# Optimization experiments

Hardware: AMD Instinct MI355X
Metric: run time of the kernel (lower is better)

Reference implementation:

```python
import jax, jax.numpy as jnp
import numpy as np

N_USER = 50000
N_ITEM = 50000
N = N_USER + N_ITEM
EMB = 64
FEAT = 64
LAYERS = [128, 128]   # input_dim = EMB + FEAT = 128
NNZ = 3_200_000
BATCH = 4096
NEG_SLOPE = 0.2
EPS = 1e-12


def setup_inputs() -> dict:
    key = jax.random.key(0)
    ks = jax.random.split(key, 16)
    inp = {}
    # forward index args
    inp["users"] = jax.random.randint(ks[0], (BATCH,), 0, N_USER)
    inp["pos_items"] = jax.random.randint(ks[1], (BATCH,), 0, N_ITEM)
    inp["neg_items"] = jax.random.randint(ks[2], (BATCH,), 0, N_ITEM)
    # learned embeddings (xavier-ish scale)
    inp["user_emb"] = jax.random.normal(ks[3], (N_USER, EMB), jnp.float32) * 0.1
    inp["item_emb1"] = jax.random.normal(ks[4], (N_ITEM, EMB), jnp.float32) * 0.1
    inp["item_emb2"] = jax.random.normal(ks[5], (N_ITEM, FEAT), jnp.float32) * 0.1
    # fixed user feature matrix (densified sparse feature, non-trainable)
    inp["feature"] = jax.random.normal(ks[6], (N_USER, FEAT), jnp.float32) * 0.1
    # hop-mixing scalar weights w1,w2,w3 (softmax(alpha) at init, then free params)
    alpha = jax.random.normal(ks[7], (3,), jnp.float32)
    inp["w"] = jax.nn.softmax(alpha)
    # per-layer GC / BI weights (all 128x128 here, so stack)
    din = EMB + FEAT
    sc = 1.0 / np.sqrt(din)
    K = len(LAYERS)
    inp["W_gc"] = jax.random.uniform(ks[8], (K, din, LAYERS[0]), jnp.float32, -sc, sc)
    inp["b_gc"] = jax.random.uniform(ks[9], (K, 1, LAYERS[0]), jnp.float32, -sc, sc)
    inp["W_bi"] = jax.random.uniform(ks[10], (K, din, LAYERS[0]), jnp.float32, -sc, sc)
    inp["b_bi"] = jax.random.uniform(ks[11], (K, 1, LAYERS[0]), jnp.float32, -sc, sc)
    # normalized adjacency in COO form (same sparsity pattern for all hops)
    inp["adj_rows"] = jax.random.randint(ks[12], (NNZ,), 0, N)
    inp["adj_cols"] = jax.random.randint(ks[13], (NNZ,), 0, N)
    inp["adj_vals"] = jax.random.uniform(ks[14], (NNZ,), jnp.float32, 0.0, 0.06)
    return inp


def _spmm(vals, rows, cols, X):
    # sparse (N,N) @ dense (N,D) via gather + segment-sum
    return jax.ops.segment_sum(vals[:, None] * X[cols], rows, num_segments=N)


def _forward(users, pos_items, neg_items, user_emb, item_emb1, item_emb2,
             feature, w, W_gc, b_gc, W_bi, b_bi, adj_rows, adj_cols, adj_vals):
    temp = jnp.concatenate([feature, item_emb2], axis=0)            # (N, FEAT)
    ego = jnp.concatenate([user_emb, item_emb1], axis=0)            # (N, EMB)
    ego = jnp.concatenate([ego, temp], axis=1)                      # (N, 128)
    all_emb = [ego]
    # torch `A ** i` cumulative -> elementwise value powers v, v^2, v^6
    v = adj_vals
    comb = w[0] * v + w[1] * (v ** 2) + w[2] * (v ** 6)
    for k in range(len(LAYERS)):
        side = _spmm(comb, adj_rows, adj_cols, ego)                 # (N, 128)
        sum_e = side @ W_gc[k] + b_gc[k]
        bi_e = (ego * side) @ W_bi[k] + b_bi[k]
        ego = jax.nn.leaky_relu(sum_e + bi_e, negative_slope=NEG_SLOPE)
        nrm = jnp.linalg.norm(ego, axis=1, keepdims=True)
        all_emb.append(ego / jnp.maximum(nrm, EPS))                 # F.normalize
    all_e = jnp.concatenate(all_emb, axis=1)                        # (N, 384)
    u_g = all_e[:N_USER][users]
    pos_g = all_e[N_USER:][pos_items]
    neg_g = all_e[N_USER:][neg_items]
    return u_g, pos_g, neg_g


def reference(users, pos_items, neg_items, user_emb, item_emb1, item_emb2,
              feature, w, W_gc, b_gc, W_bi, b_bi, adj_rows, adj_cols, adj_vals):
    return _forward(users, pos_items, neg_items, user_emb, item_emb1, item_emb2,
                    feature, w, W_gc, b_gc, W_bi, b_bi, adj_rows, adj_cols, adj_vals)
```

## Files before the change

### kernel.cpp

```cpp
#include <hip/hip_runtime.h>
#include <math.h>

#define N_USER 50000
#define N_ITEM 50000
#define NTOT   100000
#define D      128
#define BATCH_ 4096
#define NEG_SLOPE 0.2f
#define EPS_ 1e-12f
#define SCAN_CHUNK 1024
#define NBUK 782
#define NCHK 256
#define NSCAN (NBUK * NCHK)
#define BUKCAP 12288

typedef __attribute__((ext_vector_type(8))) short bfrag;
typedef __attribute__((ext_vector_type(4))) float f32x4;

static __device__ __forceinline__ float bf2f(unsigned short h) {
    return __uint_as_float(((unsigned)h) << 16);
}
static __device__ __forceinline__ unsigned short f2bf(float f) {
    unsigned u = __float_as_uint(f);
    u += 0x7fffu + ((u >> 16) & 1u);
    return (unsigned short)(u >> 16);
}

__global__ void assemble_ego0(const float* __restrict__ user_emb,
                              const float* __restrict__ item_emb1,
                              const float* __restrict__ item_emb2,
                              const float* __restrict__ feature,
                              unsigned short* __restrict__ ego0h) {
    int t = blockIdx.x * blockDim.x + threadIdx.x;
    const int total = NTOT * (D / 4);
    if (t >= total) return;
    int row = t >> 5;
    int q   = t & 31;
    int d0  = q * 4;
    const float* src;
    if (d0 < 64) {
        src = (row < N_USER) ? user_emb  + (size_t)row * 64 + d0
                             : item_emb1 + (size_t)(row - N_USER) * 64 + d0;
    } else {
        src = (row < N_USER) ? feature   + (size_t)row * 64 + (d0 - 64)
                             : item_emb2 + (size_t)(row - N_USER) * 64 + (d0 - 64);
    }
    float4 v = *(const float4*)src;
    ushort4 h;
    h.x = f2bf(v.x); h.y = f2bf(v.y); h.z = f2bf(v.z); h.w = f2bf(v.w);
    *(ushort4*)(ego0h + (size_t)row * D + d0) = h;
}

__global__ void pack_w(const float* __restrict__ W_gc, const float* __restrict__ W_bi,
                       unsigned short* __restrict__ Wp) {
    int t = blockIdx.x * blockDim.x + threadIdx.x;
    if (t >= 8192) return;
    int lane  = t & 63;
    int nt    = (t >> 6) & 7;
    int kt    = (t >> 9) & 3;
    int mat   = (t >> 11) & 1;
    int layer = (t >> 12) & 1;
    const float* W = (mat ? W_bi : W_gc) + (size_t)layer * D * D;
    int n = nt * 16 + (lane & 15);
    int kbase = kt * 32 + (lane >> 4) * 8;
    unsigned short o8[8];
    #pragma unroll
    for (int e = 0; e < 8; ++e) o8[e] = f2bf(W[(size_t)(kbase + e) * D + n]);
    *(int4*)(Wp + (size_t)t * 8) = *(int4*)o8;
}

__global__ __launch_bounds__(1024) void hist_buckets(const int* __restrict__ rows,
                                                     int* __restrict__ cnt2,
                                                     int nnz, int chunk_sz) {
    __shared__ int h[NBUK];
    for (int i = threadIdx.x; i < NBUK; i += 1024) h[i] = 0;
    __syncthreads();
    int c = blockIdx.x;
    int base = c * chunk_sz, end = min(base + chunk_sz, nnz);
    for (int e = base + threadIdx.x; e < end; e += 1024)
        atomicAdd(&h[rows[e] >> 7], 1);
    __syncthreads();
    for (int b = threadIdx.x; b < NBUK; b += 1024)
        cnt2[b * NCHK + c] = h[b];
}

__global__ __launch_bounds__(1024) void scan_block_sums(const int* __restrict__ cnt,
                                                        int* __restrict__ bsum, int n) {
    __shared__ int ws[16];
    int i = blockIdx.x * SCAN_CHUNK + threadIdx.x;
    int x = (i < n) ? cnt[i] : 0;
    #pragma unroll
    for (int d = 32; d >= 1; d >>= 1) x += __shfl_xor(x, d);
    int wid = threadIdx.x >> 6, lane = threadIdx.x & 63;
    if (lane == 0) ws[wid] = x;
    __syncthreads();
    if (threadIdx.x == 0) {
        int s = 0;
        #pragma unroll
        for (int k = 0; k < 16; ++k) s += ws[k];
        bsum[blockIdx.x] = s;
    }
}

__global__ void scan_small(const int* __restrict__ bsum, int* __restrict__ boff, int nb) {
    if (threadIdx.x == 0 && blockIdx.x == 0) {
        int acc = 0;
        for (int i = 0; i < nb; ++i) { boff[i] = acc; acc += bsum[i]; }
    }
}

__global__ __launch_bounds__(1024) void scan_chunks(const int* __restrict__ cnt,
                                                    const int* __restrict__ boff,
                                                    int* __restrict__ off, int n) {
    __shared__ int ws[16];
    int tid = threadIdx.x;
    int i = blockIdx.x * SCAN_CHUNK + tid;
    int x = (i < n) ? cnt[i] : 0;
    int v = x;
    #pragma unroll
    for (int d = 1; d < 64; d <<= 1) { int u = __shfl_up(v, d); if ((tid & 63) >= d) v += u; }
    int wid = tid >> 6, lane = tid & 63;
    if (lane == 63) ws[wid] = v;
    __syncthreads();
    if (wid == 0) {
        int s = (lane < 16) ? ws[lane] : 0;
        #pragma unroll
        for (int d = 1; d < 16; d <<= 1) { int u = __shfl_up(s, d); if (lane >= d) s += u; }
        if (lane < 16) ws[lane] = s;
    }
    __syncthreads();
    int woff = (wid == 0) ? 0 : ws[wid - 1];
    if (i < n) off[i] = boff[blockIdx.x] + woff + v - x;
}

__global__ __launch_bounds__(1024) void partition_edges(
        const int* __restrict__ rows, const int* __restrict__ cols,
        const float* __restrict__ vals, const float* __restrict__ w3,
        const int* __restrict__ scanout, int2* __restrict__ tmp8,
        int nnz, int chunk_sz) {
    __shared__ int cur[NBUK];
    int c = blockIdx.x;
    for (int b = threadIdx.x; b < NBUK; b += 1024) cur[b] = scanout[b * NCHK + c];
    __syncthreads();
    const float w0 = w3[0], w1 = w3[1], w2 = w3[2];
    int base = c * chunk_sz, end = min(base + chunk_sz, nnz);
    for (int e = base + threadIdx.x; e < end; e += 1024) {
        int r = rows[e];
        float v = vals[e];
        float v2 = v * v;
        float comb = w0 * v + w1 * v2 + w2 * v2 * v2 * v2;
        int pos = atomicAdd(&cur[r >> 7], 1);
        tmp8[pos] = make_int2(((r & 127) << 17) | cols[e], __float_as_int(comb));
    }
}

__global__ __launch_bounds__(256) void bucket_sort(
        const int2* __restrict__ tmp8, const int* __restrict__ scanout,
        unsigned* __restrict__ edges4, int* __restrict__ row_off, int nnz) {
    __shared__ int hist[128], exc[129], cur[128];
    __shared__ unsigned st[BUKCAP];
    int b = blockIdx.x;
    int lo = scanout[b * NCHK];
    int hi = (b + 1 < NBUK) ? scanout[(b + 1) * NCHK] : nnz;
    int cnt = hi - lo;
    if (threadIdx.x < 128) hist[threadIdx.x] = 0;
    __syncthreads();
    for (int i = lo + threadIdx.x; i < hi; i += 256)
        atomicAdd(&hist[tmp8[i].x >> 17], 1);
    __syncthreads();
    if (threadIdx.x == 0) {
        int a = 0;
        for (int r = 0; r < 128; ++r) { exc[r] = a; a += hist[r]; }
        exc[128] = a;
    }
    __syncthreads();
    if (threadIdx.x < 128) {
        cur[threadIdx.x] = exc[threadIdx.x];
        int grow = b * 128 + threadIdx.x;
        if (grow <= NTOT) row_off[grow] = lo + exc[threadIdx.x];
    }
    __syncthreads();
    if (cnt <= BUKCAP) {
        for (int i = lo + threadIdx.x; i < hi; i += 256) {
            int2 t = tmp8[i];
            int rl = t.x >> 17;
            int p = atomicAdd(&cur[rl], 1);
            unsigned cb = (unsigned)f2bf(__int_as_float(t.y)) & 0x7FFFu;
            st[p] = (cb << 17) | ((unsigned)t.x & 0x1FFFFu);
        }
        __syncthreads();
        for (int i = threadIdx.x; i < cnt; i += 256)
            edges4[lo + i] = st[i];
    } else {
        for (int i = lo + threadIdx.x; i < hi; i += 256) {
            int2 t = tmp8[i];
            int rl = t.x >> 17;
            int p = atomicAdd(&cur[rl], 1);
            unsigned cb = (unsigned)f2bf(__int_as_float(t.y)) & 0x7FFFu;
            edges4[lo + p] = (cb << 17) | ((unsigned)t.x & 0x1FFFFu);
        }
    }
}

__global__ __launch_bounds__(256) void spmm_csr_h(const int* __restrict__ row_off,
                                                  const unsigned* __restrict__ edges4,
                                                  const unsigned short* __restrict__ Xh,
                                                  unsigned short* __restrict__ side_h) {
    int row = (blockIdx.x * blockDim.x + threadIdx.x) >> 6;
    if (row >= NTOT) return;
    int lane = threadIdx.x & 63;
    int g = lane >> 4;
    int q = lane & 15;
    int s = row_off[row], e = row_off[row + 1];

    float a[8];
    #pragma unroll
    for (int j = 0; j < 8; ++j) a[j] = 0.f;

    for (int i = s; i < e; i += 8) {
        int i0 = i + g, i1 = i + 4 + g;
        unsigned e0 = (i0 < e) ? edges4[i0] : 0u;
        unsigned e1 = (i1 < e) ? edges4[i1] : 0u;
        float v0 = bf2f((unsigned short)(e0 >> 17));
        float v1 = bf2f((unsigned short)(e1 >> 17));
        int4 x0 = *(const int4*)(Xh + (size_t)(e0 & 0x1FFFFu) * D + q * 8);
        int4 x1 = *(const int4*)(Xh + (size_t)(e1 & 0x1FFFFu) * D + q * 8);
        const unsigned short* p0 = (const unsigned short*)&x0;
        const unsigned short* p1 = (const unsigned short*)&x1;
        #pragma unroll
        for (int j = 0; j < 8; ++j)
            a[j] += v0 * bf2f(p0[j]) + v1 * bf2f(p1[j]);
    }
    #pragma unroll
    for (int j = 0; j < 8; ++j) {
        a[j] += __shfl_xor(a[j], 16);
        a[j] += __shfl_xor(a[j], 32);
    }
    if (g == 0) {
        unsigned short o[8];
        #pragma unroll
        for (int j = 0; j < 8; ++j) o[j] = f2bf(a[j]);
        *(int4*)(side_h + (size_t)row * D + q * 8) = *(int4*)o;
    }
}

__global__ __launch_bounds__(256) void layer_gemm_mfma(
        const unsigned short* __restrict__ side_h,
        const unsigned short* __restrict__ ego_h,
        const unsigned short* __restrict__ Wp, int layer,
        const float* __restrict__ bgc, const float* __restrict__ bbi,
        unsigned short* __restrict__ ego_out_h, float* __restrict__ norms) {
    __shared__ unsigned short Sl[64 * D];
    __shared__ unsigned short Pl[64 * D];
    __shared__ float sqp[4][64];

    const int r0  = blockIdx.x * 64;
    const int tid = threadIdx.x;
    const int lane = tid & 63;
    const int wv   = tid >> 6;

    #pragma unroll
    for (int it = 0; it < 4; ++it) {
        int c = tid + it * 256;
        int r = c >> 4;
        int q = c & 15;
        int row = r0 + r;
        int4 sv = make_int4(0, 0, 0, 0), ev = make_int4(0, 0, 0, 0);
        if (row < NTOT) {
            sv = *(const int4*)(side_h + (size_t)row * D + q * 8);
            ev = *(const int4*)(ego_h  + (size_t)row * D + q * 8);
        }
        int dst = (r * 256 + q * 16) ^ ((r & 7) << 4);
        *(int4*)((char*)Sl + dst) = sv;
        const unsigned short* sp = (const unsigned short*)&sv;
        const unsigned short* ep = (const unsigned short*)&ev;
        unsigned short pv[8];
        #pragma unroll
        for (int j = 0; j < 8; ++j) pv[j] = f2bf(bf2f(sp[j]) * bf2f(ep[j]));
        *(int4*)((char*)Pl + dst) = *(int4*)pv;
    }

    bfrag wg[4][2], wb[4][2];
    #pragma unroll
    for (int kt = 0; kt < 4; ++kt)
        #pragma unroll
        for (int n2 = 0; n2 < 2; ++n2) {
            int nt = wv * 2 + n2;
            size_t og = ((((size_t)(layer * 2 + 0) * 4 + kt) * 8 + nt) * 64 + lane) * 8;
            size_t ob = ((((size_t)(layer * 2 + 1) * 4 + kt) * 8 + nt) * 64 + lane) * 8;
            wg[kt][n2] = *(const bfrag*)(Wp + og);
            wb[kt][n2] = *(const bfrag*)(Wp + ob);
        }

    __syncthreads();

    f32x4 acc[4][2];
    #pragma unroll
    for (int m = 0; m < 4; ++m)
        #pragma unroll
        for (int n = 0; n < 2; ++n) acc[m][n] = (f32x4){0.f, 0.f, 0.f, 0.f};

    #pragma unroll
    for (int kt = 0; kt < 4; ++kt) {
        bfrag sf[4], pf[4];
        #pragma unroll
        for (int m = 0; m < 4; ++m) {
            int rowl = m * 16 + (lane & 15);
            int byte = (rowl * 256 + kt * 64 + (lane >> 4) * 16) ^ ((rowl & 7) << 4);
            sf[m] = *(const bfrag*)((const char*)Sl + byte);
            pf[m] = *(const bfrag*)((const char*)Pl + byte);
        }
        #pragma unroll
        for (int m = 0; m < 4; ++m)
            #pragma unroll
            for (int n = 0; n < 2; ++n) {
                acc[m][n] = __builtin_amdgcn_mfma_f32_16x16x32_bf16(sf[m], wg[kt][n], acc[m][n], 0, 0, 0);
                acc[m][n] = __builtin_amdgcn_mfma_f32_16x16x32_bf16(pf[m], wb[kt][n], acc[m][n], 0, 0, 0);
            }
    }

    float bsum[2];
    #pragma unroll
    for (int n = 0; n < 2; ++n) {
        int col = wv * 32 + n * 16 + (lane & 15);
        bsum[n] = bgc[col] + bbi[col];
    }

    float sq[4][4];
    #pragma unroll
    for (int m = 0; m < 4; ++m)
        #pragma unroll
        for (int r = 0; r < 4; ++r) sq[m][r] = 0.f;

    #pragma unroll
    for (int m = 0; m < 4; ++m) {
        int rowl = m * 16 + (lane >> 4) * 4;
        #pragma unroll
        for (int n = 0; n < 2; ++n) {
            int col = wv * 32 + n * 16 + (lane & 15);
            #pragma unroll
            for (int r = 0; r < 4; ++r) {
                float o = acc[m][n][r] + bsum[n];
                o = (o > 0.f) ? o : NEG_SLOPE * o;
                sq[m][r] += o * o;
                int row = r0 + rowl + r;
                if (row < NTOT)
                    ego_out_h[(size_t)row * D + col] = f2bf(o);
            }
        }
    }

    #pragma unroll
    for (int m = 0; m < 4; ++m)
        #pragma unroll
        for (int r = 0; r < 4; ++r) {
            float v = sq[m][r];
            #pragma unroll
            for (int off = 8; off >= 1; off >>= 1) v += __shfl_xor(v, off);
            if ((lane & 15) == 0) sqp[wv][m * 16 + (lane >> 4) * 4 + r] = v;
        }
    __syncthreads();
    if (tid < 64) {
        int row = r0 + tid;
        if (row < NTOT) {
            float s = sqp[0][tid] + sqp[1][tid] + sqp[2][tid] + sqp[3][tid];
            norms[row] = fmaxf(sqrtf(s), EPS_);
        }
    }
}

__global__ void gather_out(const int* __restrict__ users,
                           const int* __restrict__ pos,
                           const int* __restrict__ neg,
                           const float* __restrict__ user_emb,
                           const float* __restrict__ item_emb1,
                           const float* __restrict__ item_emb2,
                           const float* __restrict__ feature,
                           const unsigned short* __restrict__ ego1h,
                           const unsigned short* __restrict__ ego2h,
                           const float* __restrict__ n1,
                           const float* __restrict__ n2,
                           float* __restrict__ out) {
    int t = blockIdx.x * blockDim.x + threadIdx.x;
    const int total = 3 * BATCH_ * 384;
    if (t >= total) return;
    int c = t % 384;
    int i = (t / 384) % BATCH_;
    int s = t / (384 * BATCH_);
    int idx  = (s == 0) ? users[i] : (s == 1 ? pos[i] : neg[i]);
    int node = (s == 0) ? idx : idx + N_USER;
    float val;
    if (c < 128) {
        if (s == 0)
            val = (c < 64) ? user_emb[(size_t)idx * 64 + c]
                           : feature[(size_t)idx * 64 + (c - 64)];
        else
            val = (c < 64) ? item_emb1[(size_t)idx * 64 + c]
                           : item_emb2[(size_t)idx * 64 + (c - 64)];
    } else if (c < 256) {
        val = bf2f(ego1h[(size_t)node * D + (c - 128)]) / n1[node];
    } else {
        val = bf2f(ego2h[(size_t)node * D + (c - 256)]) / n2[node];
    }
    out[t] = val;
}

extern "C" void kernel_launch(void* const* d_in, const int* in_sizes, int n_in,
                              void* d_out, int out_size, void* d_ws, size_t ws_size,
                              hipStream_t stream) {
    const int*   users     = (const int*)d_in[0];
    const int*   pos_items = (const int*)d_in[1];
    const int*   neg_items = (const int*)d_in[2];
    const float* user_emb  = (const float*)d_in[3];
    const float* item_emb1 = (const float*)d_in[4];
    const float* item_emb2 = (const float*)d_in[5];
    const float* feature   = (const float*)d_in[6];
    const float* w3        = (const float*)d_in[7];
    const float* W_gc      = (const float*)d_in[8];
    const float* b_gc      = (const float*)d_in[9];
    const float* W_bi      = (const float*)d_in[10];
    const float* b_bi      = (const float*)d_in[11];
    const int*   adj_rows  = (const int*)d_in[12];
    const int*   adj_cols  = (const int*)d_in[13];
    const float* adj_vals  = (const float*)d_in[14];
    const int nnz = in_sizes[14];

    const size_t nd = (size_t)NTOT * D;
    const int NB2 = (NSCAN + SCAN_CHUNK - 1) / SCAN_CHUNK;

    char* p = (char*)d_ws;
    float* n1    = (float*)p;                 p += NTOT * 4;
    float* n2    = (float*)p;                 p += NTOT * 4;
    unsigned short* ego0h  = (unsigned short*)p; p += nd * 2;
    unsigned short* ego1h  = (unsigned short*)p; p += nd * 2;
    unsigned short* ego2h  = (unsigned short*)p; p += nd * 2;
    unsigned short* side_h = (unsigned short*)p; p += nd * 2;
    unsigned short* Wp     = (unsigned short*)p; p += 8192 * 8 * 2;
    int*  row_off = (int*)p;                  p += (NTOT + 4) * 4;
    int*  cnt2    = (int*)p;                  p += (size_t)NSCAN * 4;
    int*  scanout = (int*)p;                  p += (size_t)NSCAN * 4;
    int*  bsum    = (int*)p;                  p += 256 * 4;
    int*  boff    = (int*)p;                  p += 256 * 4;
    int2* tmp8    = (int2*)p;                 p += (size_t)nnz * 8;
    unsigned* edges4 = (unsigned*)p;          p += (size_t)nnz * 4;

    float* out = (float*)d_out;

    {
        int total = NTOT * (D / 4);
        assemble_ego0<<<(total + 255) / 256, 256, 0, stream>>>(
            user_emb, item_emb1, item_emb2, feature, ego0h);
    }
    pack_w<<<8192 / 256, 256, 0, stream>>>(W_gc, W_bi, Wp);

    int chunk_sz = (nnz + NCHK - 1) / NCHK;
    hist_buckets<<<NCHK, 1024, 0, stream>>>(adj_rows, cnt2, nnz, chunk_sz);
    scan_block_sums<<<NB2, SCAN_CHUNK, 0, stream>>>(cnt2, bsum, NSCAN);
    scan_small<<<1, 64, 0, stream>>>(bsum, boff, NB2);
    scan_chunks<<<NB2, SCAN_CHUNK, 0, stream>>>(cnt2, boff, scanout, NSCAN);
    partition_edges<<<NCHK, 1024, 0, stream>>>(adj_rows, adj_cols, adj_vals, w3,
                                               scanout, tmp8, nnz, chunk_sz);
    bucket_sort<<<NBUK, 256, 0, stream>>>(tmp8, scanout, edges4, row_off, nnz);

    for (int k = 0; k < 2; ++k) {
        const unsigned short* Xh = (k == 0) ? ego0h : ego1h;
        unsigned short* egoNh    = (k == 0) ? ego1h : ego2h;
        float* nrm               = (k == 0) ? n1 : n2;

        spmm_csr_h<<<(NTOT + 3) / 4, 256, 0, stream>>>(row_off, edges4, Xh, side_h);
        layer_gemm_mfma<<<(NTOT + 63) / 64, 256, 0, stream>>>(
            side_h, Xh, Wp, k,
            b_gc + (size_t)k * D, b_bi + (size_t)k * D,
            egoNh, nrm);
    }

    {
        int total = 3 * BATCH_ * 384;
        gather_out<<<(total + 255) / 256, 256, 0, stream>>>(
            users, pos_items, neg_items,
            user_emb, item_emb1, item_emb2, feature,
            ego1h, ego2h, n1, n2, out);
    }
}
```

Measured before the change: 380.1 us.

## Fuse SpMM into layer GEMM and sort edges by column panel within rows

The separate SpMM kernel is merged into the layer GEMM kernel. Each block now gathers neighbor rows for its 64 rows and writes side and the side*ego product straight into shared memory, so the side_h round trip through global memory goes away. Separately, bucket_sort now orders edges inside each row by a column-panel key (col>>12), which groups gathers into nearby X rows for better cache locality. The sort uses more shared memory (NKEY histograms) and a halved staging buffer, which shifts more buckets onto the scattered global-write fallback. The fused kernel may also lose occupancy and parallelism because each block walks 64 rows serially.

```diff
diff --git a/kernel.cpp b/kernel.cpp
--- a/kernel.cpp
+++ b/kernel.cpp
@@ -12,7 +12,9 @@
 #define NBUK 782
 #define NCHK 256
 #define NSCAN (NBUK * NCHK)
-#define BUKCAP 12288
+#define BUKCAP 6144
+#define NPAN 25
+#define NKEY (128 * NPAN)
 
 typedef __attribute__((ext_vector_type(8))) short bfrag;
 typedef __attribute__((ext_vector_type(4))) float f32x4;
@@ -157,96 +159,78 @@
 __global__ __launch_bounds__(256) void bucket_sort(
         const int2* __restrict__ tmp8, const int* __restrict__ scanout,
         unsigned* __restrict__ edges4, int* __restrict__ row_off, int nnz) {
-    __shared__ int hist[128], exc[129], cur[128];
+    __shared__ int hist[NKEY];
+    __shared__ int cur[NKEY];
+    __shared__ int ssum[256];
+    __shared__ int wtot[4];
     __shared__ unsigned st[BUKCAP];
+    const int tid = threadIdx.x, lane = tid & 63, wv = tid >> 6;
     int b = blockIdx.x;
     int lo = scanout[b * NCHK];
     int hi = (b + 1 < NBUK) ? scanout[(b + 1) * NCHK] : nnz;
     int cnt = hi - lo;
-    if (threadIdx.x < 128) hist[threadIdx.x] = 0;
-    __syncthreads();
-    for (int i = lo + threadIdx.x; i < hi; i += 256)
-        atomicAdd(&hist[tmp8[i].x >> 17], 1);
-    __syncthreads();
-    if (threadIdx.x == 0) {
-        int a = 0;
-        for (int r = 0; r < 128; ++r) { exc[r] = a; a += hist[r]; }
-        exc[128] = a;
-    }
-    __syncthreads();
-    if (threadIdx.x < 128) {
-        cur[threadIdx.x] = exc[threadIdx.x];
-        int grow = b * 128 + threadIdx.x;
-        if (grow <= NTOT) row_off[grow] = lo + exc[threadIdx.x];
-    }
-    __syncthreads();
+
+    for (int i = tid; i < NKEY; i += 256) hist[i] = 0;
+    __syncthreads();
+    for (int i = lo + tid; i < hi; i += 256) {
+        unsigned x = (unsigned)tmp8[i].x;
+        atomicAdd(&hist[(x >> 17) * NPAN + ((x & 0x1FFFFu) >> 12)], 1);
+    }
+    __syncthreads();
+
+    const int base = tid * 13;
+    int s = 0;
+    #pragma unroll
+    for (int j = 0; j < 13; ++j) { int idx = base + j; if (idx < NKEY) s += hist[idx]; }
+    int incl = s;
+    #pragma unroll
+    for (int d = 1; d < 64; d <<= 1) { int u = __shfl_up(incl, d); if (lane >= d) incl += u; }
+    if (lane == 63) wtot[wv] = incl;
+    __syncthreads();
+    int woff = 0;
+    for (int k = 0; k < 4; ++k) if (k < wv) woff += wtot[k];
+    int acc = woff + incl - s;
+    #pragma unroll
+    for (int j = 0; j < 13; ++j) {
+        int idx = base + j;
+        if (idx < NKEY) { int h = hist[idx]; hist[idx] = acc; acc += h; }
+    }
+    __syncthreads();
+
+    for (int i = tid; i < NKEY; i += 256) cur[i] = hist[i];
+    if (tid < 128) {
+        int grow = b * 128 + tid;
+        if (grow <= NTOT) row_off[grow] = lo + hist[tid * NPAN];
+    }
+    __syncthreads();
+
     if (cnt <= BUKCAP) {
-        for (int i = lo + threadIdx.x; i < hi; i += 256) {
+        for (int i = lo + tid; i < hi; i += 256) {
             int2 t = tmp8[i];
-            int rl = t.x >> 17;
-            int p = atomicAdd(&cur[rl], 1);
+            unsigned x = (unsigned)t.x;
+            int key = (x >> 17) * NPAN + ((x & 0x1FFFFu) >> 12);
+            int p = atomicAdd(&cur[key], 1);
             unsigned cb = (unsigned)f2bf(__int_as_float(t.y)) & 0x7FFFu;
-            st[p] = (cb << 17) | ((unsigned)t.x & 0x1FFFFu);
+            st[p] = (cb << 17) | (x & 0x1FFFFu);
         }
         __syncthreads();
-        for (int i = threadIdx.x; i < cnt; i += 256)
+        for (int i = tid; i < cnt; i += 256)
             edges4[lo + i] = st[i];
     } else {
-        for (int i = lo + threadIdx.x; i < hi; i += 256) {
+        for (int i = lo + tid; i < hi; i += 256) {
             int2 t = tmp8[i];
-            int rl = t.x >> 17;
-            int p = atomicAdd(&cur[rl], 1);
+            unsigned x = (unsigned)t.x;
+            int key = (x >> 17) * NPAN + ((x & 0x1FFFFu) >> 12);
+            int p = atomicAdd(&cur[key], 1);
             unsigned cb = (unsigned)f2bf(__int_as_float(t.y)) & 0x7FFFu;
-            edges4[lo + p] = (cb << 17) | ((unsigned)t.x & 0x1FFFFu);
-        }
-    }
-}
-
-__global__ __launch_bounds__(256) void spmm_csr_h(const int* __restrict__ row_off,
-                                                  const unsigned* __restrict__ edges4,
-                                                  const unsigned short* __restrict__ Xh,
-                                                  unsigned short* __restrict__ side_h) {
-    int row = (blockIdx.x * blockDim.x + threadIdx.x) >> 6;
-    if (row >= NTOT) return;
-    int lane = threadIdx.x & 63;
-    int g = lane >> 4;
-    int q = lane & 15;
-    int s = row_off[row], e = row_off[row + 1];
-
-    float a[8];
-    #pragma unroll
-    for (int j = 0; j < 8; ++j) a[j] = 0.f;
-
-    for (int i = s; i < e; i += 8) {
-        int i0 = i + g, i1 = i + 4 + g;
-        unsigned e0 = (i0 < e) ? edges4[i0] : 0u;
-        unsigned e1 = (i1 < e) ? edges4[i1] : 0u;
-        float v0 = bf2f((unsigned short)(e0 >> 17));
-        float v1 = bf2f((unsigned short)(e1 >> 17));
-        int4 x0 = *(const int4*)(Xh + (size_t)(e0 & 0x1FFFFu) * D + q * 8);
-        int4 x1 = *(const int4*)(Xh + (size_t)(e1 & 0x1FFFFu) * D + q * 8);
-        const unsigned short* p0 = (const unsigned short*)&x0;
-        const unsigned short* p1 = (const unsigned short*)&x1;
-        #pragma unroll
-        for (int j = 0; j < 8; ++j)
-            a[j] += v0 * bf2f(p0[j]) + v1 * bf2f(p1[j]);
-    }
-    #pragma unroll
-    for (int j = 0; j < 8; ++j) {
-        a[j] += __shfl_xor(a[j], 16);
-        a[j] += __shfl_xor(a[j], 32);
-    }
-    if (g == 0) {
-        unsigned short o[8];
-        #pragma unroll
-        for (int j = 0; j < 8; ++j) o[j] = f2bf(a[j]);
-        *(int4*)(side_h + (size_t)row * D + q * 8) = *(int4*)o;
-    }
-}
-
-__global__ __launch_bounds__(256) void layer_gemm_mfma(
-        const unsigned short* __restrict__ side_h,
-        const unsigned short* __restrict__ ego_h,
+            edges4[lo + p] = (cb << 17) | (x & 0x1FFFFu);
+        }
+    }
+}
+
+__global__ __launch_bounds__(256) void layer_fused(
+        const int* __restrict__ row_off, const unsigned* __restrict__ edges4,
+        const unsigned short* __restrict__ Xh,
         const unsigned short* __restrict__ Wp, int layer,
         const float* __restrict__ bgc, const float* __restrict__ bbi,
         unsigned short* __restrict__ ego_out_h, float* __restrict__ norms) {
@@ -258,26 +242,51 @@
     const int tid = threadIdx.x;
     const int lane = tid & 63;
     const int wv   = tid >> 6;
-
-    #pragma unroll
-    for (int it = 0; it < 4; ++it) {
-        int c = tid + it * 256;
-        int r = c >> 4;
-        int q = c & 15;
-        int row = r0 + r;
-        int4 sv = make_int4(0, 0, 0, 0), ev = make_int4(0, 0, 0, 0);
+    const int g = lane >> 4;
+    const int q = lane & 15;
+
+    for (int it = 0; it < 16; ++it) {
+        int rowl = wv + it * 4;
+        int row  = r0 + rowl;
+        float a[8];
+        #pragma unroll
+        for (int j = 0; j < 8; ++j) a[j] = 0.f;
         if (row < NTOT) {
-            sv = *(const int4*)(side_h + (size_t)row * D + q * 8);
-            ev = *(const int4*)(ego_h  + (size_t)row * D + q * 8);
-        }
-        int dst = (r * 256 + q * 16) ^ ((r & 7) << 4);
-        *(int4*)((char*)Sl + dst) = sv;
-        const unsigned short* sp = (const unsigned short*)&sv;
-        const unsigned short* ep = (const unsigned short*)&ev;
-        unsigned short pv[8];
-        #pragma unroll
-        for (int j = 0; j < 8; ++j) pv[j] = f2bf(bf2f(sp[j]) * bf2f(ep[j]));
-        *(int4*)((char*)Pl + dst) = *(int4*)pv;
+            int s = row_off[row], e = row_off[row + 1];
+            for (int i = s; i < e; i += 8) {
+                int i0 = i + g, i1 = i + 4 + g;
+                unsigned e0 = (i0 < e) ? edges4[i0] : 0u;
+                unsigned e1 = (i1 < e) ? edges4[i1] : 0u;
+                float v0 = bf2f((unsigned short)(e0 >> 17));
+                float v1 = bf2f((unsigned short)(e1 >> 17));
+                int4 x0 = *(const int4*)(Xh + (size_t)(e0 & 0x1FFFFu) * D + q * 8);
+                int4 x1 = *(const int4*)(Xh + (size_t)(e1 & 0x1FFFFu) * D + q * 8);
+                const unsigned short* p0 = (const unsigned short*)&x0;
+                const unsigned short* p1 = (const unsigned short*)&x1;
+                #pragma unroll
+                for (int j = 0; j < 8; ++j)
+                    a[j] += v0 * bf2f(p0[j]) + v1 * bf2f(p1[j]);
+            }
+        }
+        #pragma unroll
+        for (int j = 0; j < 8; ++j) {
+            a[j] += __shfl_xor(a[j], 16);
+            a[j] += __shfl_xor(a[j], 32);
+        }
+        if (g == 0) {
+            int4 ev = make_int4(0, 0, 0, 0);
+            if (row < NTOT) ev = *(const int4*)(Xh + (size_t)row * D + q * 8);
+            const unsigned short* ep = (const unsigned short*)&ev;
+            unsigned short sv[8], pv[8];
+            #pragma unroll
+            for (int j = 0; j < 8; ++j) {
+                sv[j] = f2bf(a[j]);
+                pv[j] = f2bf(bf2f(sv[j]) * bf2f(ep[j]));
+            }
+            int dst = (rowl * 256 + q * 16) ^ ((rowl & 7) << 4);
+            *(int4*)((char*)Sl + dst) = *(int4*)sv;
+            *(int4*)((char*)Pl + dst) = *(int4*)pv;
+        }
     }
 
     bfrag wg[4][2], wb[4][2];
@@ -434,9 +443,8 @@
     unsigned short* ego0h  = (unsigned short*)p; p += nd * 2;
     unsigned short* ego1h  = (unsigned short*)p; p += nd * 2;
     unsigned short* ego2h  = (unsigned short*)p; p += nd * 2;
-    unsigned short* side_h = (unsigned short*)p; p += nd * 2;
     unsigned short* Wp     = (unsigned short*)p; p += 8192 * 8 * 2;
-    int*  row_off = (int*)p;                  p += (NTOT + 4) * 4;
+    int*  row_off = (int*)p;                  p += (NTOT + 128) * 4;
     int*  cnt2    = (int*)p;                  p += (size_t)NSCAN * 4;
     int*  scanout = (int*)p;                  p += (size_t)NSCAN * 4;
     int*  bsum    = (int*)p;                  p += 256 * 4;
@@ -466,10 +474,8 @@
         const unsigned short* Xh = (k == 0) ? ego0h : ego1h;
         unsigned short* egoNh    = (k == 0) ? ego1h : ego2h;
         float* nrm               = (k == 0) ? n1 : n2;
-
-        spmm_csr_h<<<(NTOT + 3) / 4, 256, 0, stream>>>(row_off, edges4, Xh, side_h);
-        layer_gemm_mfma<<<(NTOT + 63) / 64, 256, 0, stream>>>(
-            side_h, Xh, Wp, k,
+        layer_fused<<<(NTOT + 63) / 64, 256, 0, stream>>>(
+            row_off, edges4, Xh, Wp, k,
             b_gc + (size_t)k * D, b_bi + (size_t)k * D,
             egoNh, nrm);
     }
```

Result: slower. 459.0 us (+20.7%).
